# Kernel optimization log

Measured on AMD Instinct MI355X. Metric: run time of the kernel, lower is better.

The kernel has to match this reference:

```python
import jax, jax.numpy as jnp
import numpy as np

N = 100000
E = 1600000
D_IN = 64
D_OUT = 64
NUM_GRAPHS = 64
EPS = 1e-5


def setup_inputs() -> dict:
    key = jax.random.key(0)
    ks = jax.random.split(key, 8)
    x = jax.random.normal(ks[0], (N, D_IN), dtype=jnp.float32)
    edge_index = jax.random.randint(ks[1], (2, E), 0, N, dtype=jnp.int64)
    edge_attr = jax.random.uniform(ks[2], (E,), dtype=jnp.float32)
    batch_index = jnp.sort(jax.random.randint(ks[3], (N,), 0, NUM_GRAPHS, dtype=jnp.int64))
    s = 1.0 / np.sqrt(D_IN)
    W_rel = jax.random.uniform(ks[4], (D_OUT, D_IN), minval=-s, maxval=s, dtype=jnp.float32)
    b_rel = jax.random.uniform(ks[5], (D_OUT,), minval=-s, maxval=s, dtype=jnp.float32)
    W_root = jax.random.uniform(ks[6], (D_OUT, D_IN), minval=-s, maxval=s, dtype=jnp.float32)
    gn_weight = jnp.ones((D_OUT,), dtype=jnp.float32)
    gn_bias = jnp.zeros((D_OUT,), dtype=jnp.float32)
    gn_mean_scale = jnp.ones((D_OUT,), dtype=jnp.float32)
    return {"x": x, "edge_index": edge_index, "edge_attr": edge_attr,
            "batch_index": batch_index, "W_rel": W_rel, "b_rel": b_rel,
            "W_root": W_root, "gn_weight": gn_weight, "gn_bias": gn_bias,
            "gn_mean_scale": gn_mean_scale}


def reference(x, edge_index, edge_attr, batch_index, W_rel, b_rel, W_root,
              gn_weight, gn_bias, gn_mean_scale):
    src, dst = edge_index[0], edge_index[1]
    # GraphConv: out = W_rel @ sum_{j in N(i)} e_ij * x_j + W_root @ x_i + b
    msg = edge_attr[:, None] * x[src]                      # [E, D_IN]
    agg = jax.ops.segment_sum(msg, dst, num_segments=N)    # [N, D_IN]
    h = agg @ W_rel.T + b_rel + x @ W_root.T               # [N, D_OUT]
    h = jax.nn.relu(h)
    # GraphNorm over per-graph segments
    cnt = jax.ops.segment_sum(jnp.ones((N, 1), h.dtype), batch_index,
                              num_segments=NUM_GRAPHS)      # [G, 1]
    mean = jax.ops.segment_sum(h, batch_index, num_segments=NUM_GRAPHS) / cnt
    out = h - mean[batch_index] * gn_mean_scale
    var = jax.ops.segment_sum(out * out, batch_index, num_segments=NUM_GRAPHS) / cnt
    std = jnp.sqrt(var + EPS)[batch_index]
    return gn_weight * out / std + gn_bias
```

## Files before the change

kernel.cpp:

```cpp
#include <hip/hip_runtime.h>

#define N_NODES 100000
#define N_EDGES 1600000
#define D 64
#define NUM_GRAPHS 64
#define EPS 1e-5f

#define BSHIFT 9
#define NPB 512
#define NBUCKETS ((N_NODES + NPB - 1) / NPB)
#define BCAP 12288
#define A_THREADS 1024
#define A_EPT 8
#define A_CHUNK (A_THREADS * A_EPT)
#define NBLK_A ((N_EDGES + A_CHUNK - 1) / A_CHUNK)

#define SCAN_T 256
#define SCAN_E 8
#define SCAN_CHUNK (SCAN_T * SCAN_E)
#define NSCAN ((N_NODES + SCAN_CHUNK - 1) / SCAN_CHUNK)

typedef float f32x4 __attribute__((ext_vector_type(4)));
typedef short bf16x8 __attribute__((ext_vector_type(8)));

__device__ __forceinline__ ushort f32_to_bf16_rne(float v) {
    unsigned int bits = __float_as_uint(v);
    return (ushort)((bits + 0x7FFFu + ((bits >> 16) & 1u)) >> 16);
}

__global__ __launch_bounds__(256) void initA_kernel(
    int* __restrict__ bucket_cur, float* __restrict__ gsum,
    float* __restrict__ gsum2, float* __restrict__ gcnt)
{
    int i = blockIdx.x * blockDim.x + threadIdx.x;
    if (i < 256) bucket_cur[i] = i * BCAP;
    if (i < NUM_GRAPHS * 64) { gsum[i] = 0.f; gsum2[i] = 0.f; }
    if (i < 64) gcnt[i] = 0.f;
}

__global__ __launch_bounds__(256) void xcast_kernel(
    const float* __restrict__ x, ushort* __restrict__ xh)
{
    int i = blockIdx.x * blockDim.x + threadIdx.x;
    if (i >= N_NODES * 64 / 8) return;
    const float4* src = reinterpret_cast<const float4*>(x) + (size_t)i * 2;
    float4 v0 = src[0], v1 = src[1];
    float vf[8] = {v0.x, v0.y, v0.z, v0.w, v1.x, v1.y, v1.z, v1.w};
    union { ushort us[8]; uint4 u4; } o;
    #pragma unroll
    for (int j = 0; j < 8; ++j) o.us[j] = f32_to_bf16_rne(vf[j]);
    reinterpret_cast<uint4*>(xh)[i] = o.u4;
}

__global__ __launch_bounds__(A_THREADS) void binA_kernel(
    const int* __restrict__ src_idx, const int* __restrict__ dst_idx,
    const float* __restrict__ ea, int* __restrict__ bucket_cursor,
    unsigned long long* __restrict__ binned)
{
    __shared__ int hist[NBUCKETS];
    __shared__ int lbase[NBUCKETS];
    int tid = threadIdx.x;
    if (tid < NBUCKETS) hist[tid] = 0;
    __syncthreads();

    int base = blockIdx.x * A_CHUNK;
    int srcv[A_EPT], dstv[A_EPT];
    float wv[A_EPT];
    #pragma unroll
    for (int i = 0; i < A_EPT; ++i) {
        int e = base + i * A_THREADS + tid;
        if (e < N_EDGES) {
            srcv[i] = src_idx[e];
            dstv[i] = dst_idx[e];
            wv[i]   = ea[e];
            atomicAdd(&hist[dstv[i] >> BSHIFT], 1);
        } else {
            dstv[i] = -1; srcv[i] = 0; wv[i] = 0.f;
        }
    }
    __syncthreads();
    if (tid < NBUCKETS) lbase[tid] = atomicAdd(&bucket_cursor[tid], hist[tid]);
    __syncthreads();
    if (tid < NBUCKETS) hist[tid] = 0;
    __syncthreads();
    #pragma unroll
    for (int i = 0; i < A_EPT; ++i) {
        if (dstv[i] >= 0) {
            int b = dstv[i] >> BSHIFT;
            int r = atomicAdd(&hist[b], 1);
            unsigned int lo = (unsigned int)(srcv[i] | ((dstv[i] & (NPB - 1)) << 17));
            unsigned long long pv = (unsigned long long)lo |
                ((unsigned long long)__float_as_uint(wv[i]) << 32);
            binned[lbase[b] + r] = pv;
        }
    }
}

__global__ __launch_bounds__(256) void binB_kernel(
    const unsigned long long* __restrict__ binned,
    const int* __restrict__ bucket_cur,
    int2* __restrict__ offsets2, unsigned int* __restrict__ csr)
{
    __shared__ int dcnt[NPB];
    __shared__ int doff[NPB];
    __shared__ int psum[256];
    int tid = threadIdx.x;
    int b = blockIdx.x;
    int beg = b * BCAP;
    int n = bucket_cur[b] - beg;

    for (int i = tid; i < NPB; i += 256) dcnt[i] = 0;
    __syncthreads();
    for (int j = tid; j < n; j += 256) {
        unsigned long long pv = binned[beg + j];
        atomicAdd(&dcnt[((unsigned int)pv) >> 17], 1);
    }
    __syncthreads();
    int e0 = dcnt[2 * tid], e1 = dcnt[2 * tid + 1];
    psum[tid] = e0 + e1;
    __syncthreads();
    for (int off = 1; off < 256; off <<= 1) {
        int v = psum[tid];
        int a = (tid >= off) ? psum[tid - off] : 0;
        __syncthreads();
        psum[tid] = v + a;
        __syncthreads();
    }
    int ex = (tid == 0) ? 0 : psum[tid - 1];
    doff[2 * tid] = ex;
    doff[2 * tid + 1] = ex + e0;
    __syncthreads();
    for (int i = tid; i < NPB; i += 256) {
        int node = (b << BSHIFT) + i;
        if (node < N_NODES) {
            int s = beg + doff[i];
            int e = beg + ((i + 1 < NPB) ? doff[i + 1] : n);
            offsets2[node] = make_int2(s, e);
        }
        dcnt[i] = doff[i];
    }
    __syncthreads();
    for (int j = tid; j < n; j += 256) {
        unsigned long long pv = binned[beg + j];
        unsigned int lo = (unsigned int)pv;
        unsigned int wbits = (unsigned int)(pv >> 32);
        int dlo = lo >> 17;
        int r = atomicAdd(&dcnt[dlo], 1);
        unsigned int field = ((wbits + 0x7FFFu + ((wbits >> 16) & 1u)) >> 16) & 0x7FFFu;
        csr[beg + r] = (lo & 0x1FFFFu) | (field << 17);
    }
}

__global__ __launch_bounds__(256) void gatherh_kernel(
    const ushort* __restrict__ xh, const int2* __restrict__ offsets2,
    const unsigned int* __restrict__ csr, ushort* __restrict__ agg)
{
    int wid = (int)((blockIdx.x * blockDim.x + threadIdx.x) >> 6);
    if (wid >= N_NODES) return;
    int lane = threadIdx.x & 63;
    int2 o2 = offsets2[wid];
    int beg = __builtin_amdgcn_readfirstlane(o2.x);
    int end = __builtin_amdgcn_readfirstlane(o2.y);
    float acc[8];
    #pragma unroll
    for (int u = 0; u < 8; ++u) acc[u] = 0.f;
    int j = beg;
    for (; j + 7 < end; j += 8) {
        unsigned int e[8];
        #pragma unroll
        for (int u = 0; u < 8; ++u) e[u] = csr[j + u];
        float xv[8];
        #pragma unroll
        for (int u = 0; u < 8; ++u)
            xv[u] = __uint_as_float((unsigned int)xh[(size_t)(e[u] & 0x1FFFFu) * 64 + lane] << 16);
        #pragma unroll
        for (int u = 0; u < 8; ++u)
            acc[u] = fmaf(__uint_as_float((e[u] >> 17) << 16), xv[u], acc[u]);
    }
    for (; j < end; ++j) {
        unsigned int e0 = csr[j];
        float xv = __uint_as_float((unsigned int)xh[(size_t)(e0 & 0x1FFFFu) * 64 + lane] << 16);
        acc[0] = fmaf(__uint_as_float((e0 >> 17) << 16), xv, acc[0]);
    }
    float a = ((acc[0] + acc[1]) + (acc[2] + acc[3])) +
              ((acc[4] + acc[5]) + (acc[6] + acc[7]));
    agg[(size_t)wid * 64 + lane] = f32_to_bf16_rne(a);
}

#define DB 128
__global__ __launch_bounds__(256) void dense_mfma16_kernel(
    const ushort* __restrict__ agg, const ushort* __restrict__ xh,
    ushort* __restrict__ hout,
    const float* __restrict__ W_rel, const float* __restrict__ b_rel,
    const float* __restrict__ W_root)
{
    __shared__ unsigned int Bf[4][4][64][4];
    int tid = threadIdx.x;

    #pragma unroll
    for (int g = 0; g < 8; ++g) {
        int q = tid * 8 + g;
        int i4   = (q & 1) * 4;
        int lane = (q >> 1) & 63;
        int dt   = (q >> 7) & 3;
        int kt   = (q >> 9) & 3;
        int d = dt * 16 + (lane & 15);
        int k = kt * 32 + (lane >> 4) * 8 + i4;
        const float* Wsrc = (k < 64) ? (W_rel + d * 64 + k)
                                     : (W_root + d * 64 + (k - 64));
        float4 w = *reinterpret_cast<const float4*>(Wsrc);
        unsigned int b0 = f32_to_bf16_rne(w.x);
        unsigned int b1 = f32_to_bf16_rne(w.y);
        unsigned int b2 = f32_to_bf16_rne(w.z);
        unsigned int b3 = f32_to_bf16_rne(w.w);
        int u = i4 >> 1;
        Bf[kt][dt][lane][u]     = b0 | (b1 << 16);
        Bf[kt][dt][lane][u + 1] = b2 | (b3 << 16);
    }
    __syncthreads();

    int wid = tid >> 6, lane = tid & 63;
    int nbase = blockIdx.x * DB + wid * 32;
    int r = lane & 15;
    int k0 = (lane >> 4) * 8;

    f32x4 acc[2][4];
    #pragma unroll
    for (int nt = 0; nt < 2; ++nt)
        #pragma unroll
        for (int dt = 0; dt < 4; ++dt)
            acc[nt][dt] = (f32x4){0.f, 0.f, 0.f, 0.f};

    bf16x8 zf;
    #pragma unroll
    for (int i = 0; i < 8; ++i) zf[i] = 0;

    #pragma unroll 1
    for (int kt = 0; kt < 4; ++kt) {
        bf16x8 bh[4];
        #pragma unroll
        for (int dt = 0; dt < 4; ++dt)
            bh[dt] = *reinterpret_cast<const bf16x8*>(&Bf[kt][dt][lane][0]);
        int kk = kt * 32 + k0;
        #pragma unroll
        for (int nt = 0; nt < 2; ++nt) {
            int node = nbase + nt * 16 + r;
            bool ok = (node < N_NODES);
            const ushort* srcrow = (kk < 64)
                ? (agg + (size_t)node * 64 + kk)
                : (xh + (size_t)node * 64 + (kk - 64));
            bf16x8 a = ok ? *reinterpret_cast<const bf16x8*>(srcrow) : zf;
            #pragma unroll
            for (int dt = 0; dt < 4; ++dt)
                acc[nt][dt] = __builtin_amdgcn_mfma_f32_16x16x32_bf16(a, bh[dt], acc[nt][dt], 0, 0, 0);
        }
    }

    int rowg = (lane >> 4) * 4;
    #pragma unroll
    for (int dt = 0; dt < 4; ++dt) {
        int d = dt * 16 + r;
        float bias = b_rel[d];
        #pragma unroll
        for (int nt = 0; nt < 2; ++nt) {
            #pragma unroll
            for (int reg = 0; reg < 4; ++reg) {
                int node = nbase + nt * 16 + rowg + reg;
                if (node < N_NODES) {
                    float v = fmaxf(acc[nt][dt][reg] + bias, 0.f);
                    hout[(size_t)node * 64 + d] = f32_to_bf16_rne(v);
                }
            }
        }
    }
}

#define NPW 32
__global__ __launch_bounds__(256) void stats16_kernel(
    const ushort* __restrict__ h,
    const int* __restrict__ batch,
    float* __restrict__ gsum,
    float* __restrict__ gsum2,
    float* __restrict__ gcnt)
{
    int wave = (int)((blockIdx.x * blockDim.x + threadIdx.x) >> 6);
    int lane = threadIdx.x & 63;
    int base = wave * NPW;
    if (base >= N_NODES) return;
    int end = min(base + NPW, N_NODES);

    int gcur = batch[base];
    float s = 0.f, s2 = 0.f, cnt = 0.f;
    for (int n = base; n < end; ++n) {
        int g = batch[n];
        if (g != gcur) {
            atomicAdd(&gsum[gcur * 64 + lane], s);
            atomicAdd(&gsum2[gcur * 64 + lane], s2);
            if (lane == 0) atomicAdd(&gcnt[gcur], cnt);
            s = 0.f; s2 = 0.f; cnt = 0.f;
            gcur = g;
        }
        float v = __uint_as_float((unsigned int)h[(size_t)n * 64 + lane] << 16);
        s += v;
        s2 = fmaf(v, v, s2);
        cnt += 1.f;
    }
    atomicAdd(&gsum[gcur * 64 + lane], s);
    atomicAdd(&gsum2[gcur * 64 + lane], s2);
    if (lane == 0) atomicAdd(&gcnt[gcur], cnt);
}

__global__ __launch_bounds__(256) void finalize_kernel(
    const float* __restrict__ gsum,
    const float* __restrict__ gsum2,
    const float* __restrict__ gcnt,
    const float* __restrict__ gn_w,
    const float* __restrict__ gn_b,
    const float* __restrict__ gn_ms,
    float* __restrict__ Ag,
    float* __restrict__ Bg)
{
    int i = blockIdx.x * blockDim.x + threadIdx.x;
    if (i >= NUM_GRAPHS * 64) return;
    int g = i >> 6, d = i & 63;
    float c = fmaxf(gcnt[g], 1.f);
    float m = gsum[i] / c;
    float q = gsum2[i] / c;
    float s = gn_ms[d];
    float var = q - (2.f * s - s * s) * m * m;
    float inv = rsqrtf(fmaxf(var, 0.f) + EPS);
    float A = gn_w[d] * inv;
    Ag[i] = A;
    Bg[i] = gn_b[d] - A * s * m;
}

__global__ __launch_bounds__(256) void apply16_kernel(
    const ushort* __restrict__ h,
    const int* __restrict__ batch,
    const float* __restrict__ Ag,
    const float* __restrict__ Bg,
    float* __restrict__ out)
{
    int i = blockIdx.x * blockDim.x + threadIdx.x;
    if (i >= N_NODES * 8) return;
    int n = i >> 3;
    int q = i & 7;
    int g = batch[n];
    union { uint4 u4; ushort us[8]; } hv;
    hv.u4 = *reinterpret_cast<const uint4*>(h + (size_t)n * 64 + q * 8);
    const float4* Av = reinterpret_cast<const float4*>(Ag + g * 64 + q * 8);
    const float4* Bv = reinterpret_cast<const float4*>(Bg + g * 64 + q * 8);
    float4 A0 = Av[0], A1 = Av[1];
    float4 B0 = Bv[0], B1 = Bv[1];
    float Af[8] = {A0.x, A0.y, A0.z, A0.w, A1.x, A1.y, A1.z, A1.w};
    float Bf_[8] = {B0.x, B0.y, B0.z, B0.w, B1.x, B1.y, B1.z, B1.w};
    float4 o0, o1;
    float of[8];
    #pragma unroll
    for (int j = 0; j < 8; ++j) {
        float v = __uint_as_float((unsigned int)hv.us[j] << 16);
        of[j] = fmaf(Af[j], v, Bf_[j]);
    }
    o0.x = of[0]; o0.y = of[1]; o0.z = of[2]; o0.w = of[3];
    o1.x = of[4]; o1.y = of[5]; o1.z = of[6]; o1.w = of[7];
    float4* op = reinterpret_cast<float4*>(out + (size_t)n * 64 + q * 8);
    op[0] = o0;
    op[1] = o1;
}

__global__ __launch_bounds__(256) void hist_kernel(
    const int* __restrict__ dst_idx, int* __restrict__ deg)
{
    int e = blockIdx.x * blockDim.x + threadIdx.x;
    if (e >= N_EDGES) return;
    atomicAdd(&deg[dst_idx[e]], 1);
}

__global__ __launch_bounds__(SCAN_T) void scan1_kernel(
    const int* __restrict__ deg, int* __restrict__ offsets,
    int* __restrict__ blocksum)
{
    __shared__ int lds[SCAN_T];
    int b = blockIdx.x, t = threadIdx.x;
    int base = b * SCAN_CHUNK + t * SCAN_E;
    int v[SCAN_E];
    int s = 0;
    #pragma unroll
    for (int i = 0; i < SCAN_E; ++i) {
        v[i] = (base + i < N_NODES) ? deg[base + i] : 0;
        s += v[i];
    }
    lds[t] = s;
    __syncthreads();
    for (int off = 1; off < SCAN_T; off <<= 1) {
        int val = lds[t];
        int add = (t >= off) ? lds[t - off] : 0;
        __syncthreads();
        lds[t] = val + add;
        __syncthreads();
    }
    if (t == SCAN_T - 1) blocksum[b] = lds[SCAN_T - 1];
    int run = (t == 0) ? 0 : lds[t - 1];
    #pragma unroll
    for (int i = 0; i < SCAN_E; ++i) {
        if (base + i < N_NODES) offsets[base + i] = run;
        run += v[i];
    }
}

__global__ __launch_bounds__(64) void scan2_kernel(
    const int* __restrict__ blocksum, int* __restrict__ blockoff)
{
    __shared__ int lds[64];
    int t = threadIdx.x;
    lds[t] = (t < NSCAN) ? blocksum[t] : 0;
    __syncthreads();
    for (int off = 1; off < 64; off <<= 1) {
        int val = lds[t];
        int add = (t >= off) ? lds[t - off] : 0;
        __syncthreads();
        lds[t] = val + add;
        __syncthreads();
    }
    if (t < NSCAN) blockoff[t] = (t == 0) ? 0 : lds[t - 1];
}

__global__ __launch_bounds__(256) void scan3_kernel(
    int* __restrict__ offsets, const int* __restrict__ blockoff,
    int* __restrict__ cursor)
{
    int i = blockIdx.x * blockDim.x + threadIdx.x;
    if (i < N_NODES) {
        int v = offsets[i] + blockoff[i / SCAN_CHUNK];
        offsets[i] = v;
        cursor[i] = v;
    }
    if (i == 0) offsets[N_NODES] = N_EDGES;
}

__global__ __launch_bounds__(256) void fill_kernel(
    const int* __restrict__ src_idx, const int* __restrict__ dst_idx,
    const float* __restrict__ ea, int* __restrict__ cursor,
    int2* __restrict__ csr)
{
    int e = blockIdx.x * blockDim.x + threadIdx.x;
    if (e >= N_EDGES) return;
    int s = src_idx[e];
    int d = dst_idx[e];
    float w = ea[e];
    int pos = atomicAdd(&cursor[d], 1);
    csr[pos] = make_int2(s, __float_as_int(w));
}

__global__ __launch_bounds__(256) void gather_kernel(
    const float* __restrict__ x, const int* __restrict__ offsets,
    const int2* __restrict__ csr, float* __restrict__ agg)
{
    int wid = (int)((blockIdx.x * blockDim.x + threadIdx.x) >> 6);
    if (wid >= N_NODES) return;
    int lane = threadIdx.x & 63;
    int beg = __builtin_amdgcn_readfirstlane(offsets[wid]);
    int end = __builtin_amdgcn_readfirstlane(offsets[wid + 1]);
    float acc0 = 0.f, acc1 = 0.f;
    int j = beg;
    for (; j + 1 < end; j += 2) {
        int2 a = csr[j];
        int2 b = csr[j + 1];
        acc0 = fmaf(__int_as_float(a.y), x[(size_t)a.x * 64 + lane], acc0);
        acc1 = fmaf(__int_as_float(b.y), x[(size_t)b.x * 64 + lane], acc1);
    }
    if (j < end) {
        int2 a = csr[j];
        acc0 = fmaf(__int_as_float(a.y), x[(size_t)a.x * 64 + lane], acc0);
    }
    agg[(size_t)wid * 64 + lane] = acc0 + acc1;
}

__global__ __launch_bounds__(256) void scatter_kernel(
    const float* __restrict__ x,
    const int* __restrict__ src_idx,
    const int* __restrict__ dst_idx,
    const float* __restrict__ ea,
    float* __restrict__ agg)
{
    long long gid = (long long)blockIdx.x * blockDim.x + threadIdx.x;
    if (gid >= (long long)N_EDGES * 16) return;
    int e = (int)(gid >> 4);
    int q = (int)(gid & 15);
    int s = src_idx[e];
    int d = dst_idx[e];
    float w = ea[e];
    float4 v = reinterpret_cast<const float4*>(x)[(size_t)s * 16 + q];
    float* out = agg + (size_t)d * 64 + q * 4;
    atomicAdd(out + 0, w * v.x);
    atomicAdd(out + 1, w * v.y);
    atomicAdd(out + 2, w * v.z);
    atomicAdd(out + 3, w * v.w);
}

__global__ __launch_bounds__(256) void dense_mfma_kernel(
    float* __restrict__ aggh,
    const float* __restrict__ x,
    const float* __restrict__ W_rel,
    const float* __restrict__ b_rel,
    const float* __restrict__ W_root)
{
    __shared__ unsigned int Bf[2][4][4][64][4];
    int tid = threadIdx.x;
    #pragma unroll
    for (int g = 0; g < 8; ++g) {
        int q = tid * 8 + g;
        int i4   = (q & 1) * 4;
        int lane = (q >> 1) & 63;
        int dt   = (q >> 7) & 3;
        int kt   = (q >> 9) & 3;
        int d = dt * 16 + (lane & 15);
        int k = kt * 32 + (lane >> 4) * 8 + i4;
        const float* Wsrc = (k < 64) ? (W_rel + d * 64 + k)
                                     : (W_root + d * 64 + (k - 64));
        float4 w = *reinterpret_cast<const float4*>(Wsrc);
        float wf[4] = {w.x, w.y, w.z, w.w};
        unsigned int hi[4], lo[4];
        #pragma unroll
        for (int j = 0; j < 4; ++j) {
            unsigned int bits = __float_as_uint(wf[j]);
            hi[j] = bits >> 16;
            float resid = wf[j] - __uint_as_float(bits & 0xFFFF0000u);
            lo[j] = __float_as_uint(resid) >> 16;
        }
        int u = i4 >> 1;
        Bf[0][kt][dt][lane][u]     = hi[0] | (hi[1] << 16);
        Bf[0][kt][dt][lane][u + 1] = hi[2] | (hi[3] << 16);
        Bf[1][kt][dt][lane][u]     = lo[0] | (lo[1] << 16);
        Bf[1][kt][dt][lane][u + 1] = lo[2] | (lo[3] << 16);
    }
    __syncthreads();

    int wid = tid >> 6, lane = tid & 63;
    int nbase = blockIdx.x * DB + wid * 32;
    int r = lane & 15;
    int k0 = (lane >> 4) * 8;

    f32x4 acc[2][4];
    #pragma unroll
    for (int nt = 0; nt < 2; ++nt)
        #pragma unroll
        for (int dt = 0; dt < 4; ++dt)
            acc[nt][dt] = (f32x4){0.f, 0.f, 0.f, 0.f};

    #pragma unroll 1
    for (int kt = 0; kt < 4; ++kt) {
        bf16x8 bh[4], bl[4];
        #pragma unroll
        for (int dt = 0; dt < 4; ++dt) {
            bh[dt] = *reinterpret_cast<const bf16x8*>(&Bf[0][kt][dt][lane][0]);
            bl[dt] = *reinterpret_cast<const bf16x8*>(&Bf[1][kt][dt][lane][0]);
        }
        int kk = kt * 32 + k0;
        #pragma unroll
        for (int nt = 0; nt < 2; ++nt) {
            int node = nbase + nt * 16 + r;
            float av[8];
            if (node < N_NODES) {
                const float* srcrow = (kk < 64)
                    ? (aggh + (size_t)node * 64 + kk)
                    : (x + (size_t)node * 64 + (kk - 64));
                float4 v0 = reinterpret_cast<const float4*>(srcrow)[0];
                float4 v1 = reinterpret_cast<const float4*>(srcrow)[1];
                av[0] = v0.x; av[1] = v0.y; av[2] = v0.z; av[3] = v0.w;
                av[4] = v1.x; av[5] = v1.y; av[6] = v1.z; av[7] = v1.w;
            } else {
                #pragma unroll
                for (int i = 0; i < 8; ++i) av[i] = 0.f;
            }
            bf16x8 ah, al;
            #pragma unroll
            for (int i = 0; i < 8; ++i) {
                unsigned int bits = __float_as_uint(av[i]);
                ah[i] = (short)(bits >> 16);
                float resid = av[i] - __uint_as_float(bits & 0xFFFF0000u);
                al[i] = (short)(__float_as_uint(resid) >> 16);
            }
            #pragma unroll
            for (int dt = 0; dt < 4; ++dt) {
                acc[nt][dt] = __builtin_amdgcn_mfma_f32_16x16x32_bf16(ah, bh[dt], acc[nt][dt], 0, 0, 0);
                acc[nt][dt] = __builtin_amdgcn_mfma_f32_16x16x32_bf16(al, bh[dt], acc[nt][dt], 0, 0, 0);
                acc[nt][dt] = __builtin_amdgcn_mfma_f32_16x16x32_bf16(ah, bl[dt], acc[nt][dt], 0, 0, 0);
            }
        }
    }

    int rowg = (lane >> 4) * 4;
    #pragma unroll
    for (int dt = 0; dt < 4; ++dt) {
        int d = dt * 16 + r;
        float bias = b_rel[d];
        #pragma unroll
        for (int nt = 0; nt < 2; ++nt) {
            #pragma unroll
            for (int reg = 0; reg < 4; ++reg) {
                int node = nbase + nt * 16 + rowg + reg;
                if (node < N_NODES) {
                    float v = fmaxf(acc[nt][dt][reg] + bias, 0.f);
                    aggh[(size_t)node * 64 + d] = v;
                }
            }
        }
    }
}

__global__ __launch_bounds__(256) void stats_kernel(
    const float* __restrict__ h,
    const int* __restrict__ batch,
    float* __restrict__ gsum,
    float* __restrict__ gsum2,
    float* __restrict__ gcnt)
{
    int wave = (int)((blockIdx.x * blockDim.x + threadIdx.x) >> 6);
    int lane = threadIdx.x & 63;
    int base = wave * NPW;
    if (base >= N_NODES) return;
    int end = min(base + NPW, N_NODES);

    int gcur = batch[base];
    float s = 0.f, s2 = 0.f, cnt = 0.f;
    for (int n = base; n < end; ++n) {
        int g = batch[n];
        if (g != gcur) {
            atomicAdd(&gsum[gcur * 64 + lane], s);
            atomicAdd(&gsum2[gcur * 64 + lane], s2);
            if (lane == 0) atomicAdd(&gcnt[gcur], cnt);
            s = 0.f; s2 = 0.f; cnt = 0.f;
            gcur = g;
        }
        float v = h[(size_t)n * 64 + lane];
        s += v;
        s2 = fmaf(v, v, s2);
        cnt += 1.f;
    }
    atomicAdd(&gsum[gcur * 64 + lane], s);
    atomicAdd(&gsum2[gcur * 64 + lane], s2);
    if (lane == 0) atomicAdd(&gcnt[gcur], cnt);
}

__global__ __launch_bounds__(256) void apply_kernel(
    const float* __restrict__ h,
    const int* __restrict__ batch,
    const float* __restrict__ Ag,
    const float* __restrict__ Bg,
    float* __restrict__ out)
{
    long long gid = (long long)blockIdx.x * blockDim.x + threadIdx.x;
    if (gid >= (long long)N_NODES * 16) return;
    int n = (int)(gid >> 4);
    int q = (int)(gid & 15);
    int g = batch[n];
    float4 hv = reinterpret_cast<const float4*>(h)[gid];
    float4 A = reinterpret_cast<const float4*>(Ag)[g * 16 + q];
    float4 B = reinterpret_cast<const float4*>(Bg)[g * 16 + q];
    float4 o;
    o.x = fmaf(A.x, hv.x, B.x);
    o.y = fmaf(A.y, hv.y, B.y);
    o.z = fmaf(A.z, hv.z, B.z);
    o.w = fmaf(A.w, hv.w, B.w);
    reinterpret_cast<float4*>(out)[gid] = o;
}

extern "C" void kernel_launch(void* const* d_in, const int* in_sizes, int n_in,
                              void* d_out, int out_size, void* d_ws, size_t ws_size,
                              hipStream_t stream)
{
    const float* x      = (const float*)d_in[0];
    const int*   ei     = (const int*)d_in[1];
    const float* ea     = (const float*)d_in[2];
    const int*   batch  = (const int*)d_in[3];
    const float* W_rel  = (const float*)d_in[4];
    const float* b_rel  = (const float*)d_in[5];
    const float* W_root = (const float*)d_in[6];
    const float* gn_w   = (const float*)d_in[7];
    const float* gn_b   = (const float*)d_in[8];
    const float* gn_ms  = (const float*)d_in[9];
    const int* src_idx = ei;
    const int* dst_idx = ei + N_EDGES;

    char* wsp = (char*)d_ws;

    int*   bucket_cur  = (int*)wsp;
    float* gsumN       = (float*)(bucket_cur + 256);
    float* gsum2N      = gsumN + NUM_GRAPHS * 64;
    float* gcntN       = gsum2N + NUM_GRAPHS * 64;
    int2*  offsets2    = (int2*)(gcntN + 64);
    size_t regA_off    = (((size_t)((char*)(offsets2 + N_NODES) - wsp)) + 15) & ~(size_t)15;
    size_t binned_sz   = (size_t)NBUCKETS * BCAP * 8;
    size_t hbuf_sz     = (size_t)N_NODES * 64 * 2;
    size_t regA_sz     = (binned_sz > hbuf_sz ? binned_sz : hbuf_sz);
    unsigned long long* binned = (unsigned long long*)(wsp + regA_off);
    ushort* hbuf16     = (ushort*)(wsp + regA_off);
    unsigned int* csrN = (unsigned int*)(wsp + regA_off + regA_sz);
    ushort* aggN       = (ushort*)((char*)csrN + (size_t)NBUCKETS * BCAP * 4);
    float*  AgN        = (float*)(aggN + (size_t)N_NODES * 64);
    float*  BgN        = AgN + NUM_GRAPHS * 64;
    ushort* xh         = (ushort*)(BgN + NUM_GRAPHS * 64);
    size_t reqN        = (size_t)((char*)(xh + (size_t)N_NODES * 64) - wsp);

    int*   degL     = (int*)wsp;
    float* gsumL    = (float*)(degL + N_NODES);
    float* gsum2L   = gsumL + NUM_GRAPHS * 64;
    float* gcntL    = gsum2L + NUM_GRAPHS * 64;
    size_t zeroL    = ((size_t)N_NODES + 2 * NUM_GRAPHS * 64 + 64) * 4;
    int*   offsetsL = (int*)(gcntL + 64);
    int*   blocksum = offsetsL + N_NODES + 1;
    int*   blockoff = blocksum + 64;
    int*   cursorL  = blockoff + 64;
    size_t csrL_off = (((size_t)((char*)(cursorL + N_NODES) - wsp)) + 15) & ~(size_t)15;
    int2*  csrL     = (int2*)(wsp + csrL_off);
    float* aggL     = (float*)(csrL + N_EDGES);
    float* AgL      = aggL + (size_t)N_NODES * 64;
    float* BgL      = AgL + NUM_GRAPHS * 64;
    size_t reqL     = (size_t)((char*)(BgL + NUM_GRAPHS * 64) - wsp);

    if (ws_size >= reqN) {
        initA_kernel<<<(NUM_GRAPHS * 64 + 255) / 256, 256, 0, stream>>>(
            bucket_cur, gsumN, gsum2N, gcntN);
        xcast_kernel<<<(N_NODES * 64 / 8 + 255) / 256, 256, 0, stream>>>(x, xh);
        binA_kernel<<<NBLK_A, A_THREADS, 0, stream>>>(src_idx, dst_idx, ea, bucket_cur, binned);
        binB_kernel<<<NBUCKETS, 256, 0, stream>>>(binned, bucket_cur, offsets2, csrN);
        gatherh_kernel<<<(N_NODES + 3) / 4, 256, 0, stream>>>(xh, offsets2, csrN, aggN);
        dense_mfma16_kernel<<<(N_NODES + DB - 1) / DB, 256, 0, stream>>>(
            aggN, xh, hbuf16, W_rel, b_rel, W_root);
        {
            int waves = (N_NODES + NPW - 1) / NPW;
            stats16_kernel<<<(waves + 3) / 4, 256, 0, stream>>>(hbuf16, batch, gsumN, gsum2N, gcntN);
        }
        finalize_kernel<<<(NUM_GRAPHS * 64 + 255) / 256, 256, 0, stream>>>(
            gsumN, gsum2N, gcntN, gn_w, gn_b, gn_ms, AgN, BgN);
        apply16_kernel<<<(N_NODES * 8 + 255) / 256, 256, 0, stream>>>(
            hbuf16, batch, AgN, BgN, (float*)d_out);
    } else if (ws_size >= reqL) {
        hipMemsetAsync(d_ws, 0, zeroL, stream);
        hist_kernel<<<(N_EDGES + 255) / 256, 256, 0, stream>>>(dst_idx, degL);
        scan1_kernel<<<NSCAN, SCAN_T, 0, stream>>>(degL, offsetsL, blocksum);
        scan2_kernel<<<1, 64, 0, stream>>>(blocksum, blockoff);
        scan3_kernel<<<(N_NODES + 255) / 256, 256, 0, stream>>>(offsetsL, blockoff, cursorL);
        fill_kernel<<<(N_EDGES + 255) / 256, 256, 0, stream>>>(src_idx, dst_idx, ea, cursorL, csrL);
        gather_kernel<<<(N_NODES + 3) / 4, 256, 0, stream>>>(x, offsetsL, csrL, aggL);
        dense_mfma_kernel<<<(N_NODES + DB - 1) / DB, 256, 0, stream>>>(
            aggL, x, W_rel, b_rel, W_root);
        {
            int waves = (N_NODES + NPW - 1) / NPW;
            stats_kernel<<<(waves + 3) / 4, 256, 0, stream>>>(aggL, batch, gsumL, gsum2L, gcntL);
        }
        finalize_kernel<<<(NUM_GRAPHS * 64 + 255) / 256, 256, 0, stream>>>(
            gsumL, gsum2L, gcntL, gn_w, gn_b, gn_ms, AgL, BgL);
        {
            long long total = (long long)N_NODES * 16;
            apply_kernel<<<(int)((total + 255) / 256), 256, 0, stream>>>(
                aggL, batch, AgL, BgL, (float*)d_out);
        }
    } else {
        float* agg = (float*)(gcntL + 64);
        float* Ag  = agg + (size_t)N_NODES * 64;
        float* Bg  = Ag + NUM_GRAPHS * 64;
        size_t zb = zeroL + (size_t)N_NODES * 64 * 4;
        hipMemsetAsync(d_ws, 0, zb, stream);
        long long total = (long long)N_EDGES * 16;
        scatter_kernel<<<(int)((total + 255) / 256), 256, 0, stream>>>(
            x, src_idx, dst_idx, ea, agg);
        dense_mfma_kernel<<<(N_NODES + DB - 1) / DB, 256, 0, stream>>>(
            agg, x, W_rel, b_rel, W_root);
        {
            int waves = (N_NODES + NPW - 1) / NPW;
            stats_kernel<<<(waves + 3) / 4, 256, 0, stream>>>(agg, batch, gsumL, gsum2L, gcntL);
        }
        finalize_kernel<<<(NUM_GRAPHS * 64 + 255) / 256, 256, 0, stream>>>(
            gsumL, gsum2L, gcntL, gn_w, gn_b, gn_ms, Ag, Bg);
        {
            long long t2 = (long long)N_NODES * 16;
            apply_kernel<<<(int)((t2 + 255) / 256), 256, 0, stream>>>(
                agg, batch, Ag, Bg, (float*)d_out);
        }
    }
}
```

Baseline: 157.8 us.

## Fuse GraphNorm statistics into dense MFMA epilogue and merge init with xcast

Folds the per-graph sum and sum-of-squares accumulation into the dense MFMA kernel's epilogue. Each block reduces into shared memory per graph and then issues global atomics, which removes the separate stats kernel and its re-read of h. The init kernel is also merged into the xcast kernel as extra blocks, saving one launch. In exchange, the epilogue now performs many shared-memory atomics per element, which could contend and lengthen the dense kernel.

```diff
diff --git a/kernel.cpp b/kernel.cpp
--- a/kernel.cpp
+++ b/kernel.cpp
@@ -14,6 +14,7 @@
 #define A_EPT 8
 #define A_CHUNK (A_THREADS * A_EPT)
 #define NBLK_A ((N_EDGES + A_CHUNK - 1) / A_CHUNK)
+#define XB ((N_NODES * 64 / 8 + 255) / 256)
 
 #define SCAN_T 256
 #define SCAN_E 8
@@ -28,28 +29,27 @@
     return (ushort)((bits + 0x7FFFu + ((bits >> 16) & 1u)) >> 16);
 }
 
-__global__ __launch_bounds__(256) void initA_kernel(
+__global__ __launch_bounds__(256) void xcast_init_kernel(
+    const float* __restrict__ x, ushort* __restrict__ xh,
     int* __restrict__ bucket_cur, float* __restrict__ gsum,
     float* __restrict__ gsum2, float* __restrict__ gcnt)
 {
-    int i = blockIdx.x * blockDim.x + threadIdx.x;
-    if (i < 256) bucket_cur[i] = i * BCAP;
-    if (i < NUM_GRAPHS * 64) { gsum[i] = 0.f; gsum2[i] = 0.f; }
-    if (i < 64) gcnt[i] = 0.f;
-}
-
-__global__ __launch_bounds__(256) void xcast_kernel(
-    const float* __restrict__ x, ushort* __restrict__ xh)
-{
-    int i = blockIdx.x * blockDim.x + threadIdx.x;
-    if (i >= N_NODES * 64 / 8) return;
-    const float4* src = reinterpret_cast<const float4*>(x) + (size_t)i * 2;
-    float4 v0 = src[0], v1 = src[1];
-    float vf[8] = {v0.x, v0.y, v0.z, v0.w, v1.x, v1.y, v1.z, v1.w};
-    union { ushort us[8]; uint4 u4; } o;
-    #pragma unroll
-    for (int j = 0; j < 8; ++j) o.us[j] = f32_to_bf16_rne(vf[j]);
-    reinterpret_cast<uint4*>(xh)[i] = o.u4;
+    if (blockIdx.x < XB) {
+        int i = blockIdx.x * blockDim.x + threadIdx.x;
+        if (i >= N_NODES * 64 / 8) return;
+        const float4* src = reinterpret_cast<const float4*>(x) + (size_t)i * 2;
+        float4 v0 = src[0], v1 = src[1];
+        float vf[8] = {v0.x, v0.y, v0.z, v0.w, v1.x, v1.y, v1.z, v1.w};
+        union { ushort us[8]; uint4 u4; } o;
+        #pragma unroll
+        for (int j = 0; j < 8; ++j) o.us[j] = f32_to_bf16_rne(vf[j]);
+        reinterpret_cast<uint4*>(xh)[i] = o.u4;
+    } else {
+        int i = (blockIdx.x - XB) * 256 + threadIdx.x;
+        if (i < 256) bucket_cur[i] = i * BCAP;
+        if (i < NUM_GRAPHS * 64) { gsum[i] = 0.f; gsum2[i] = 0.f; }
+        if (i < 64) gcnt[i] = 0.f;
+    }
 }
 
 __global__ __launch_bounds__(A_THREADS) void binA_kernel(
@@ -188,14 +188,22 @@
 }
 
 #define DB 128
-__global__ __launch_bounds__(256) void dense_mfma16_kernel(
+__global__ __launch_bounds__(256) void dense_mfma16_stats_kernel(
     const ushort* __restrict__ agg, const ushort* __restrict__ xh,
     ushort* __restrict__ hout,
     const float* __restrict__ W_rel, const float* __restrict__ b_rel,
-    const float* __restrict__ W_root)
+    const float* __restrict__ W_root,
+    const int* __restrict__ batch,
+    float* __restrict__ gsum, float* __restrict__ gsum2,
+    float* __restrict__ gcnt)
 {
     __shared__ unsigned int Bf[4][4][64][4];
+    __shared__ float ls[8][64];
+    __shared__ float ls2[8][64];
+    __shared__ int lcnt[8];
+    __shared__ int ginfo[2];
     int tid = threadIdx.x;
+    int nbase = blockIdx.x * DB;
 
     #pragma unroll
     for (int g = 0; g < 8; ++g) {
@@ -217,10 +225,18 @@
         Bf[kt][dt][lane][u]     = b0 | (b1 << 16);
         Bf[kt][dt][lane][u + 1] = b2 | (b3 << 16);
     }
+    for (int i = tid; i < 8 * 64; i += 256) { ls[i >> 6][i & 63] = 0.f; ls2[i >> 6][i & 63] = 0.f; }
+    if (tid < 8) lcnt[tid] = 0;
+    if (tid == 0) {
+        int gb = batch[nbase];
+        int last = min(nbase + DB - 1, N_NODES - 1);
+        ginfo[0] = gb;
+        ginfo[1] = batch[last] - gb + 1;
+    }
     __syncthreads();
 
     int wid = tid >> 6, lane = tid & 63;
-    int nbase = blockIdx.x * DB + wid * 32;
+    int wbase = nbase + wid * 32;
     int r = lane & 15;
     int k0 = (lane >> 4) * 8;
 
@@ -244,7 +260,7 @@
         int kk = kt * 32 + k0;
         #pragma unroll
         for (int nt = 0; nt < 2; ++nt) {
-            int node = nbase + nt * 16 + r;
+            int node = wbase + nt * 16 + r;
             bool ok = (node < N_NODES);
             const ushort* srcrow = (kk < 64)
                 ? (agg + (size_t)node * 64 + kk)
@@ -256,58 +272,62 @@
         }
     }
 
+    int gbase = ginfo[0];
+    bool fits = (ginfo[1] <= 8);
+    float bias[4];
+    #pragma unroll
+    for (int dt = 0; dt < 4; ++dt) bias[dt] = b_rel[dt * 16 + r];
+
     int rowg = (lane >> 4) * 4;
     #pragma unroll
-    for (int dt = 0; dt < 4; ++dt) {
-        int d = dt * 16 + r;
-        float bias = b_rel[d];
-        #pragma unroll
-        for (int nt = 0; nt < 2; ++nt) {
-            #pragma unroll
-            for (int reg = 0; reg < 4; ++reg) {
-                int node = nbase + nt * 16 + rowg + reg;
-                if (node < N_NODES) {
-                    float v = fmaxf(acc[nt][dt][reg] + bias, 0.f);
-                    hout[(size_t)node * 64 + d] = f32_to_bf16_rne(v);
+    for (int nt = 0; nt < 2; ++nt) {
+        #pragma unroll
+        for (int reg = 0; reg < 4; ++reg) {
+            int node = wbase + nt * 16 + rowg + reg;
+            if (node < N_NODES) {
+                int g = batch[node];
+                int gs = g - gbase;
+                #pragma unroll
+                for (int dt = 0; dt < 4; ++dt) {
+                    int d = dt * 16 + r;
+                    float v = fmaxf(acc[nt][dt][reg] + bias[dt], 0.f);
+                    ushort hb = f32_to_bf16_rne(v);
+                    hout[(size_t)node * 64 + d] = hb;
+                    float vr = __uint_as_float((unsigned int)hb << 16);
+                    if (fits) {
+                        atomicAdd(&ls[gs][d], vr);
+                        atomicAdd(&ls2[gs][d], vr * vr);
+                    } else {
+                        atomicAdd(&gsum[g * 64 + d], vr);
+                        atomicAdd(&gsum2[g * 64 + d], vr * vr);
+                    }
                 }
             }
         }
     }
-}
-
-#define NPW 32
-__global__ __launch_bounds__(256) void stats16_kernel(
-    const ushort* __restrict__ h,
-    const int* __restrict__ batch,
-    float* __restrict__ gsum,
-    float* __restrict__ gsum2,
-    float* __restrict__ gcnt)
-{
-    int wave = (int)((blockIdx.x * blockDim.x + threadIdx.x) >> 6);
-    int lane = threadIdx.x & 63;
-    int base = wave * NPW;
-    if (base >= N_NODES) return;
-    int end = min(base + NPW, N_NODES);
-
-    int gcur = batch[base];
-    float s = 0.f, s2 = 0.f, cnt = 0.f;
-    for (int n = base; n < end; ++n) {
-        int g = batch[n];
-        if (g != gcur) {
-            atomicAdd(&gsum[gcur * 64 + lane], s);
-            atomicAdd(&gsum2[gcur * 64 + lane], s2);
-            if (lane == 0) atomicAdd(&gcnt[gcur], cnt);
-            s = 0.f; s2 = 0.f; cnt = 0.f;
-            gcur = g;
-        }
-        float v = __uint_as_float((unsigned int)h[(size_t)n * 64 + lane] << 16);
-        s += v;
-        s2 = fmaf(v, v, s2);
-        cnt += 1.f;
-    }
-    atomicAdd(&gsum[gcur * 64 + lane], s);
-    atomicAdd(&gsum2[gcur * 64 + lane], s2);
-    if (lane == 0) atomicAdd(&gcnt[gcur], cnt);
+    if (tid < DB) {
+        int node = nbase + tid;
+        if (node < N_NODES) {
+            int g = batch[node];
+            if (fits) atomicAdd(&lcnt[g - gbase], 1);
+            else atomicAdd(&gcnt[g], 1.f);
+        }
+    }
+    __syncthreads();
+    if (fits) {
+        int gspan = ginfo[1];
+        for (int i = tid; i < gspan * 64; i += 256) {
+            int gs = i >> 6, d = i & 63;
+            float s = ls[gs][d];
+            float s2 = ls2[gs][d];
+            if (s != 0.f || s2 != 0.f) {
+                atomicAdd(&gsum[(gbase + gs) * 64 + d], s);
+                atomicAdd(&gsum2[(gbase + gs) * 64 + d], s2);
+            }
+        }
+        if (tid < gspan && lcnt[tid] > 0)
+            atomicAdd(&gcnt[gbase + tid], (float)lcnt[tid]);
+    }
 }
 
 __global__ __launch_bounds__(256) void finalize_kernel(
@@ -609,6 +629,7 @@
     }
 }
 
+#define NPW 32
 __global__ __launch_bounds__(256) void stats_kernel(
     const float* __restrict__ h,
     const int* __restrict__ batch,
@@ -720,18 +741,13 @@
     size_t reqL     = (size_t)((char*)(BgL + NUM_GRAPHS * 64) - wsp);
 
     if (ws_size >= reqN) {
-        initA_kernel<<<(NUM_GRAPHS * 64 + 255) / 256, 256, 0, stream>>>(
-            bucket_cur, gsumN, gsum2N, gcntN);
-        xcast_kernel<<<(N_NODES * 64 / 8 + 255) / 256, 256, 0, stream>>>(x, xh);
+        xcast_init_kernel<<<XB + 16, 256, 0, stream>>>(
+            x, xh, bucket_cur, gsumN, gsum2N, gcntN);
         binA_kernel<<<NBLK_A, A_THREADS, 0, stream>>>(src_idx, dst_idx, ea, bucket_cur, binned);
         binB_kernel<<<NBUCKETS, 256, 0, stream>>>(binned, bucket_cur, offsets2, csrN);
         gatherh_kernel<<<(N_NODES + 3) / 4, 256, 0, stream>>>(xh, offsets2, csrN, aggN);
-        dense_mfma16_kernel<<<(N_NODES + DB - 1) / DB, 256, 0, stream>>>(
-            aggN, xh, hbuf16, W_rel, b_rel, W_root);
-        {
-            int waves = (N_NODES + NPW - 1) / NPW;
-            stats16_kernel<<<(waves + 3) / 4, 256, 0, stream>>>(hbuf16, batch, gsumN, gsum2N, gcntN);
-        }
+        dense_mfma16_stats_kernel<<<(N_NODES + DB - 1) / DB, 256, 0, stream>>>(
+            aggN, xh, hbuf16, W_rel, b_rel, W_root, batch, gsumN, gsum2N, gcntN);
         finalize_kernel<<<(NUM_GRAPHS * 64 + 255) / 256, 256, 0, stream>>>(
             gsumN, gsum2N, gcntN, gn_w, gn_b, gn_ms, AgN, BgN);
         apply16_kernel<<<(N_NODES * 8 + 255) / 256, 256, 0, stream>>>(
```

Measured after the change: 199.1 us. 1.26x slower.
